# Optimization experiments

Hardware: AMD Instinct MI355X
Metric: run time of the kernel (lower is better)

The kernel has to match this reference:

```python
import jax, jax.numpy as jnp
import numpy as np

N_SRC, N_DST, N_EDGES = 60000, 50000, 600000
IN_DIM, OUT_DIM = 256, 128


def setup_inputs() -> dict:
    key = jax.random.key(0)
    k1, k2, k3, k4, k5, k6 = jax.random.split(key, 6)
    features = jax.random.normal(k1, (N_SRC, IN_DIM), dtype=jnp.float32)
    t = jax.random.uniform(k2, (N_SRC,), dtype=jnp.float32)
    edge_src = jax.random.randint(k3, (N_EDGES,), 0, N_SRC, dtype=jnp.int32)
    edge_dst = jax.random.randint(k4, (N_EDGES,), 0, N_DST, dtype=jnp.int32)
    # learned params: xavier_normal with relu gain for fc, default for temporal_fc
    gain = float(np.sqrt(2.0))
    std_fc = gain * np.sqrt(2.0 / (IN_DIM + OUT_DIM))
    W_fc = jax.random.normal(k5, (OUT_DIM, IN_DIM), dtype=jnp.float32) * std_fc
    W_t = jax.random.normal(k6, (1, OUT_DIM), dtype=jnp.float32) * (1.0 / np.sqrt(OUT_DIM))
    return {"features": features, "t": t, "edge_src": edge_src,
            "edge_dst": edge_dst, "n_dst": N_DST, "W_fc": W_fc, "W_t": W_t}


def reference(features, t, edge_src, edge_dst, n_dst, W_fc, W_t):
    # z = fc(h), no bias
    z = features @ W_fc.T                      # [n_src, out_dim]
    s = (z @ W_t.T)[:, 0]                      # temporal_fc(z) -> [n_src]
    # edge attention: e = -|t_src - t_dst| (non-differentiable in original)
    e = jax.lax.stop_gradient(-jnp.abs(t[edge_src] - t[edge_dst]))  # [E]
    # mailbox logits: exp(temporal_fc(z_src) * e / 500)
    y = jnp.exp(s[edge_src] * e / 500.0)       # [E]
    # segment softmax over incoming edges of each dst node
    m = jax.ops.segment_max(y, edge_dst, num_segments=n_dst)
    m = jnp.where(jnp.isfinite(m), m, 0.0)     # empty mailboxes
    ex = jnp.exp(y - m[edge_dst])
    denom = jax.ops.segment_sum(ex, edge_dst, num_segments=n_dst)
    alpha = ex / denom[edge_dst]               # [E]
    # weighted neighbor sum
    h = jax.ops.segment_sum(alpha[:, None] * z[edge_src], edge_dst, num_segments=n_dst)
    # residual
    return z[:n_dst] + h
```

## Files before the change

kernel.cpp:

```cpp
#include <hip/hip_runtime.h>
#include <cstdint>

#define NBINS 1024
#define EPB   4096
#define MAXE  1536

typedef __attribute__((ext_vector_type(8))) _Float16 half8;
typedef __attribute__((ext_vector_type(4))) float floatx4;

__device__ __forceinline__ half8 gload16(const void* p) {
    half8 v;
    asm volatile("global_load_dwordx4 %0, %1, off" : "=v"(v) : "v"(p));
    return v;
}

__global__ __launch_bounds__(512, 4) void gemm_hist(
    const float* __restrict__ A, const float* __restrict__ W,
    const float* __restrict__ Wt, const int* __restrict__ edst,
    _Float16* __restrict__ z16, float* __restrict__ s,
    int* __restrict__ gcount, int M, int E, int NBH)
{
    __shared__ __align__(16) unsigned char smem[65536];

    if ((int)blockIdx.x < NBH) {
        int* h = (int*)smem;
        for (int i = threadIdx.x; i < NBINS; i += 512) h[i] = 0;
        __syncthreads();
        int base = blockIdx.x * EPB + threadIdx.x * 8;
        if (base + 8 <= E) {
            int4 d0 = *(const int4*)(edst + base);
            int4 d1 = *(const int4*)(edst + base + 4);
            atomicAdd(&h[d0.x >> 6], 1); atomicAdd(&h[d0.y >> 6], 1);
            atomicAdd(&h[d0.z >> 6], 1); atomicAdd(&h[d0.w >> 6], 1);
            atomicAdd(&h[d1.x >> 6], 1); atomicAdd(&h[d1.y >> 6], 1);
            atomicAdd(&h[d1.z >> 6], 1); atomicAdd(&h[d1.w >> 6], 1);
        } else {
            for (int i = 0; i < 8; ++i)
                if (base + i < E) atomicAdd(&h[edst[base + i] >> 6], 1);
        }
        __syncthreads();
        for (int i = threadIdx.x; i < NBINS; i += 512)
            gcount[(size_t)blockIdx.x * NBINS + i] = h[i];
        return;
    }

    half8* Wlds = (half8*)smem;
    const int tile = blockIdx.x - NBH;
    const int tid  = threadIdx.x;
    const int lane = tid & 63;
    const int w    = tid >> 6;
    const int m    = lane & 15;
    const int q    = lane >> 4;

#pragma unroll
    for (int it = 0; it < 8; ++it) {
        int pair = w * 8 + it;
        int nt = pair & 7, ks = pair >> 3;
        const float* src = W + (size_t)(nt * 16 + m) * 256 + ks * 32 + q * 8;
        float4 w0 = *(const float4*)src;
        float4 w1 = *(const float4*)(src + 4);
        half8 h;
        h[0] = (_Float16)w0.x; h[1] = (_Float16)w0.y;
        h[2] = (_Float16)w0.z; h[3] = (_Float16)w0.w;
        h[4] = (_Float16)w1.x; h[5] = (_Float16)w1.y;
        h[6] = (_Float16)w1.z; h[7] = (_Float16)w1.w;
        Wlds[pair * 64 + lane] = h;
    }

    const int row_base = tile * 128 + w * 16;
    const int arow = min(row_base + m, M - 1);
    const float* ap = A + (size_t)arow * 256 + q * 8;

    float4 abuf[8];
#pragma unroll
    for (int i = 0; i < 4; ++i) {
        abuf[2 * i]     = *(const float4*)(ap + i * 32);
        abuf[2 * i + 1] = *(const float4*)(ap + i * 32 + 4);
    }

    floatx4 acc[8];
#pragma unroll
    for (int nt = 0; nt < 8; ++nt) acc[nt] = (floatx4){0.f, 0.f, 0.f, 0.f};

    __syncthreads();

#pragma unroll
    for (int ks = 0; ks < 8; ++ks) {
        float4 a0 = abuf[(ks & 3) * 2];
        float4 a1 = abuf[(ks & 3) * 2 + 1];
        half8 af;
        af[0] = (_Float16)a0.x; af[1] = (_Float16)a0.y;
        af[2] = (_Float16)a0.z; af[3] = (_Float16)a0.w;
        af[4] = (_Float16)a1.x; af[5] = (_Float16)a1.y;
        af[6] = (_Float16)a1.z; af[7] = (_Float16)a1.w;

        if (ks < 4) {
            abuf[(ks & 3) * 2]     = *(const float4*)(ap + (ks + 4) * 32);
            abuf[(ks & 3) * 2 + 1] = *(const float4*)(ap + (ks + 4) * 32 + 4);
        }

#pragma unroll
        for (int nt = 0; nt < 8; ++nt) {
            half8 bf = Wlds[(ks * 8 + nt) * 64 + lane];
            acc[nt] = __builtin_amdgcn_mfma_f32_16x16x32_f16(
                af, bf, acc[nt], 0, 0, 0);
        }
    }

    float wt[8];
#pragma unroll
    for (int nt = 0; nt < 8; ++nt) wt[nt] = Wt[nt * 16 + m];

    float sp[4] = {0.f, 0.f, 0.f, 0.f};
#pragma unroll
    for (int nt = 0; nt < 8; ++nt)
#pragma unroll
        for (int reg = 0; reg < 4; ++reg)
            sp[reg] += acc[nt][reg] * wt[nt];

#pragma unroll
    for (int reg = 0; reg < 4; ++reg) {
        int row = row_base + q * 4 + reg;
        if (row < M) {
#pragma unroll
            for (int nt = 0; nt < 8; ++nt)
                z16[(size_t)row * 128 + nt * 16 + m] = (_Float16)acc[nt][reg];
        }
    }
#pragma unroll
    for (int off = 1; off <= 8; off <<= 1)
#pragma unroll
        for (int reg = 0; reg < 4; ++reg)
            sp[reg] += __shfl_xor(sp[reg], off, 64);
    if (m == 0) {
#pragma unroll
        for (int reg = 0; reg < 4; ++reg) {
            int row = row_base + q * 4 + reg;
            if (row < M) s[row] = sp[reg];
        }
    }
}

__global__ __launch_bounds__(256) void part_scan(
    int* __restrict__ gcount, int* __restrict__ binTot, int NB)
{
    int b    = blockIdx.x * 4 + (threadIdx.x >> 6);
    int lane = threadIdx.x & 63;
    if (b >= NBINS) return;
    int chunks = (NB + 63) >> 6;
    int run = 0;
    for (int c = 0; c < chunks; ++c) {
        int blk = c * 64 + lane;
        int v = (blk < NB) ? gcount[(size_t)blk * NBINS + b] : 0;
        int incl = v;
#pragma unroll
        for (int off = 1; off < 64; off <<= 1) {
            int n = __shfl_up(incl, off, 64);
            if (lane >= off) incl += n;
        }
        if (blk < NB) gcount[(size_t)blk * NBINS + b] = run + incl - v;
        run += __shfl(incl, 63, 64);
    }
    if (lane == 0) binTot[b] = run;
}

__global__ __launch_bounds__(1024) void part_scanB(
    const int* __restrict__ binTot, int* __restrict__ binstart)
{
    __shared__ int wsum[16];
    int b = threadIdx.x;
    int lane = b & 63, wv = b >> 6;
    int v = binTot[b];
    int x = v;
#pragma unroll
    for (int off = 1; off < 64; off <<= 1) {
        int n = __shfl_up(x, off, 64);
        if (lane >= off) x += n;
    }
    if (lane == 63) wsum[wv] = x;
    __syncthreads();
    if (b < 64) {
        int t = (b < 16) ? wsum[b] : 0;
#pragma unroll
        for (int off = 1; off < 16; off <<= 1) {
            int n = __shfl_up(t, off, 64);
            if (lane >= off) t += n;
        }
        if (b < 16) wsum[b] = t;
    }
    __syncthreads();
    int base = (wv > 0) ? wsum[wv - 1] : 0;
    binstart[b] = base + x - v;
    if (b == NBINS - 1) binstart[NBINS] = base + x;
}

__global__ __launch_bounds__(512) void part_scatter(
    const int* __restrict__ esrc, const int* __restrict__ edst,
    const float* __restrict__ t, const float* __restrict__ s,
    const int* __restrict__ gcount, const int* __restrict__ binstart,
    int2* __restrict__ part, int E)
{
    __shared__ int hloc[NBINS];
    __shared__ int hbase[NBINS];
    for (int i = threadIdx.x; i < NBINS; i += 512) hloc[i] = 0;
    __syncthreads();

    int base = blockIdx.x * EPB + threadIdx.x * 8;
    int si[8], di[8], rk[8];
    int nv = 0;
    if (base < E) {
        nv = E - base; if (nv > 8) nv = 8;
        if (nv == 8) {
            int4 s0 = *(const int4*)(esrc + base);
            int4 s1 = *(const int4*)(esrc + base + 4);
            int4 d0 = *(const int4*)(edst + base);
            int4 d1 = *(const int4*)(edst + base + 4);
            si[0]=s0.x; si[1]=s0.y; si[2]=s0.z; si[3]=s0.w;
            si[4]=s1.x; si[5]=s1.y; si[6]=s1.z; si[7]=s1.w;
            di[0]=d0.x; di[1]=d0.y; di[2]=d0.z; di[3]=d0.w;
            di[4]=d1.x; di[5]=d1.y; di[6]=d1.z; di[7]=d1.w;
        } else {
            for (int i = 0; i < 8; ++i) {
                int e = min(base + i, E - 1);
                si[i] = esrc[e]; di[i] = edst[e];
            }
        }
#pragma unroll
        for (int i = 0; i < 8; ++i)
            if (i < nv) rk[i] = atomicAdd(&hloc[di[i] >> 6], 1);
    }

    for (int i = threadIdx.x; i < NBINS; i += 512)
        hbase[i] = binstart[i] + gcount[(size_t)blockIdx.x * NBINS + i];
    __syncthreads();

#pragma unroll
    for (int i = 0; i < 8; ++i) {
        if (i < nv) {
            float ee = -fabsf(t[si[i]] - t[di[i]]);
            float exv = __expf(__expf(s[si[i]] * ee * (1.0f / 500.0f)));
            part[hbase[di[i] >> 6] + rk[i]] =
                make_int2((si[i] & 0xffff) | ((di[i] & 63) << 16),
                          __float_as_int(exv));
        }
    }
}

__global__ __launch_bounds__(256) void aggregate(
    const _Float16* __restrict__ z16, const int* __restrict__ binstart,
    const int2* __restrict__ part, float* __restrict__ out, int Nd)
{
    __shared__ int2 arr[MAXE];
    __shared__ int lcnt[64];
    __shared__ int loff[65];

    const int tid = threadIdx.x;
    const int b = blockIdx.x;
    const int s0 = binstart[b];
    int nE = binstart[b + 1] - s0;
    if (nE > MAXE) nE = MAXE;

    if (tid < 64) lcnt[tid] = 0;
    __syncthreads();

    int2 rec[6]; int rrk[6], rloc[6], nrec = 0;
    for (int i = tid; i < nE; i += 256) {
        int2 r = part[s0 + i];
        int loc = (r.x >> 16) & 63;
        rec[nrec] = r;
        rloc[nrec] = loc;
        rrk[nrec] = atomicAdd(&lcnt[loc], 1);
        ++nrec;
    }
    __syncthreads();
    if (tid < 64) {
        int v = lcnt[tid], x = v;
#pragma unroll
        for (int off = 1; off < 64; off <<= 1) {
            int n = __shfl_up(x, off, 64);
            if (tid >= off) x += n;
        }
        loff[tid + 1] = x;
        if (tid == 0) loff[0] = 0;
    }
    __syncthreads();
    for (int i = 0; i < nrec; ++i)
        arr[loff[rloc[i]] + rrk[i]] = rec[i];
    __syncthreads();

    const int g = tid >> 4;
    const int l = tid & 15;

#pragma unroll 1
    for (int pass = 0; pass < 4; ++pass) {
        const int loc = pass * 16 + g;
        const int jb = loff[loc], je = loff[loc + 1];

        float acc[8];
#pragma unroll
        for (int i = 0; i < 8; ++i) acc[i] = 0.f;
        float ds = 0.f;

        for (int j = jb; j < je; j += 8) {
            float x[8];
            const void* p[8];
#pragma unroll
            for (int k = 0; k < 8; ++k) {
                bool vk = (j + k) < je;
                int jj = vk ? (j + k) : (je - 1);
                int2 r = arr[jj];
                x[k] = vk ? __int_as_float(r.y) : 0.f;
                p[k] = (const void*)(z16 + (size_t)(r.x & 0xffff) * 128 + l * 8);
            }
            half8 v0 = gload16(p[0]);
            half8 v1 = gload16(p[1]);
            half8 v2 = gload16(p[2]);
            half8 v3 = gload16(p[3]);
            half8 v4 = gload16(p[4]);
            half8 v5 = gload16(p[5]);
            half8 v6 = gload16(p[6]);
            half8 v7 = gload16(p[7]);
            asm volatile("s_waitcnt vmcnt(0)" ::: "memory");
            __builtin_amdgcn_sched_barrier(0);
            ds += ((x[0] + x[1]) + (x[2] + x[3])) +
                  ((x[4] + x[5]) + (x[6] + x[7]));
#pragma unroll
            for (int i = 0; i < 8; ++i) {
                acc[i] = fmaf(x[0], (float)v0[i], acc[i]);
                acc[i] = fmaf(x[1], (float)v1[i], acc[i]);
                acc[i] = fmaf(x[2], (float)v2[i], acc[i]);
                acc[i] = fmaf(x[3], (float)v3[i], acc[i]);
                acc[i] = fmaf(x[4], (float)v4[i], acc[i]);
                acc[i] = fmaf(x[5], (float)v5[i], acc[i]);
                acc[i] = fmaf(x[6], (float)v6[i], acc[i]);
                acc[i] = fmaf(x[7], (float)v7[i], acc[i]);
            }
        }

        int d = b * 64 + loc;
        if (d < Nd) {
            float inv = (je > jb) ? 1.0f / ds : 0.0f;
            const half8* zr = (const half8*)(z16 + (size_t)d * 128 + l * 8);
            half8 r0 = *zr;
            float* op = out + (size_t)d * 128 + l * 8;
            *(float4*)(op + 0) = make_float4(fmaf(acc[0], inv, (float)r0[0]),
                                             fmaf(acc[1], inv, (float)r0[1]),
                                             fmaf(acc[2], inv, (float)r0[2]),
                                             fmaf(acc[3], inv, (float)r0[3]));
            *(float4*)(op + 4) = make_float4(fmaf(acc[4], inv, (float)r0[4]),
                                             fmaf(acc[5], inv, (float)r0[5]),
                                             fmaf(acc[6], inv, (float)r0[6]),
                                             fmaf(acc[7], inv, (float)r0[7]));
        }
    }
}

extern "C" void kernel_launch(void* const* d_in, const int* in_sizes, int n_in,
                              void* d_out, int out_size, void* d_ws, size_t ws_size,
                              hipStream_t stream)
{
    const float* features = (const float*)d_in[0];
    const float* t        = (const float*)d_in[1];
    const int*   esrc     = (const int*)d_in[2];
    const int*   edst     = (const int*)d_in[3];
    const float* Wfc      = (const float*)d_in[5];
    const float* Wt       = (const float*)d_in[6];
    float* out = (float*)d_out;

    const int M  = in_sizes[1];
    const int E  = in_sizes[2];
    const int OD = in_sizes[6];
    const int Nd = out_size / OD;

    const int NBH = (E + EPB - 1) / EPB;
    const int GB  = (M + 127) / 128;

    _Float16* z16      = (_Float16*)d_ws;
    float*    s        = (float*)(z16 + (size_t)M * 128);
    int*      gcount   = (int*)(s + M);
    int*      binTot   = gcount + (size_t)NBH * NBINS;
    int*      binstart = binTot + NBINS;
    int2*     part     = (int2*)(binstart + NBINS + 4);

    gemm_hist<<<NBH + GB, 512, 0, stream>>>(features, Wfc, Wt, edst,
                                            z16, s, gcount, M, E, NBH);
    part_scan<<<NBINS / 4, 256, 0, stream>>>(gcount, binTot, NBH);
    part_scanB<<<1, 1024, 0, stream>>>(binTot, binstart);
    part_scatter<<<NBH, 512, 0, stream>>>(esrc, edst, t, s, gcount, binstart,
                                          part, E);
    aggregate<<<(Nd + 63) / 64, 256, 0, stream>>>(z16, binstart, part, out, Nd);
}
```

Measured before the change: 174.4 us.

## Split z16 into four column panels and process panels sequentially in aggregate

```diff
diff --git a/kernel.cpp b/kernel.cpp
--- a/kernel.cpp
+++ b/kernel.cpp
@@ -124,7 +124,8 @@
         if (row < M) {
 #pragma unroll
             for (int nt = 0; nt < 8; ++nt)
-                z16[(size_t)row * 128 + nt * 16 + m] = (_Float16)acc[nt][reg];
+                z16[(size_t)(nt >> 1) * (size_t)M * 32 +
+                    (size_t)row * 32 + (nt & 1) * 16 + m] = (_Float16)acc[nt][reg];
         }
     }
 #pragma unroll
@@ -248,7 +249,7 @@
 
 __global__ __launch_bounds__(256) void aggregate(
     const _Float16* __restrict__ z16, const int* __restrict__ binstart,
-    const int2* __restrict__ part, float* __restrict__ out, int Nd)
+    const int2* __restrict__ part, float* __restrict__ out, int M, int Nd)
 {
     __shared__ int2 arr[MAXE];
     __shared__ int lcnt[64];
@@ -288,42 +289,44 @@
         arr[loff[rloc[i]] + rrk[i]] = rec[i];
     __syncthreads();
 
-    const int g = tid >> 4;
-    const int l = tid & 15;
+    const int slot = tid >> 2;
+    const int f    = tid & 3;
+    const int jb = loff[slot], je = loff[slot + 1];
+    const int d  = b * 64 + slot;
+    float dsv = 0.f;
 
 #pragma unroll 1
-    for (int pass = 0; pass < 4; ++pass) {
-        const int loc = pass * 16 + g;
-        const int jb = loff[loc], je = loff[loc + 1];
+    for (int p = 0; p < 4; ++p) {
+        const _Float16* zp = z16 + (size_t)p * (size_t)M * 32;
 
         float acc[8];
 #pragma unroll
         for (int i = 0; i < 8; ++i) acc[i] = 0.f;
-        float ds = 0.f;
 
         for (int j = jb; j < je; j += 8) {
             float x[8];
-            const void* p[8];
+            const void* pp[8];
 #pragma unroll
             for (int k = 0; k < 8; ++k) {
                 bool vk = (j + k) < je;
                 int jj = vk ? (j + k) : (je - 1);
                 int2 r = arr[jj];
                 x[k] = vk ? __int_as_float(r.y) : 0.f;
-                p[k] = (const void*)(z16 + (size_t)(r.x & 0xffff) * 128 + l * 8);
+                pp[k] = (const void*)(zp + (size_t)(r.x & 0xffff) * 32 + f * 8);
             }
-            half8 v0 = gload16(p[0]);
-            half8 v1 = gload16(p[1]);
-            half8 v2 = gload16(p[2]);
-            half8 v3 = gload16(p[3]);
-            half8 v4 = gload16(p[4]);
-            half8 v5 = gload16(p[5]);
-            half8 v6 = gload16(p[6]);
-            half8 v7 = gload16(p[7]);
+            half8 v0 = gload16(pp[0]);
+            half8 v1 = gload16(pp[1]);
+            half8 v2 = gload16(pp[2]);
+            half8 v3 = gload16(pp[3]);
+            half8 v4 = gload16(pp[4]);
+            half8 v5 = gload16(pp[5]);
+            half8 v6 = gload16(pp[6]);
+            half8 v7 = gload16(pp[7]);
             asm volatile("s_waitcnt vmcnt(0)" ::: "memory");
             __builtin_amdgcn_sched_barrier(0);
-            ds += ((x[0] + x[1]) + (x[2] + x[3])) +
-                  ((x[4] + x[5]) + (x[6] + x[7]));
+            if (p == 0)
+                dsv += ((x[0] + x[1]) + (x[2] + x[3])) +
+                       ((x[4] + x[5]) + (x[6] + x[7]));
 #pragma unroll
             for (int i = 0; i < 8; ++i) {
                 acc[i] = fmaf(x[0], (float)v0[i], acc[i]);
@@ -337,12 +340,10 @@
             }
         }
 
-        int d = b * 64 + loc;
         if (d < Nd) {
-            float inv = (je > jb) ? 1.0f / ds : 0.0f;
-            const half8* zr = (const half8*)(z16 + (size_t)d * 128 + l * 8);
-            half8 r0 = *zr;
-            float* op = out + (size_t)d * 128 + l * 8;
+            float inv = (je > jb) ? 1.0f / dsv : 0.0f;
+            half8 r0 = *(const half8*)(zp + (size_t)d * 32 + f * 8);
+            float* op = out + (size_t)d * 128 + p * 32 + f * 8;
             *(float4*)(op + 0) = make_float4(fmaf(acc[0], inv, (float)r0[0]),
                                              fmaf(acc[1], inv, (float)r0[1]),
                                              fmaf(acc[2], inv, (float)r0[2]),
@@ -388,5 +389,6 @@
     part_scanB<<<1, 1024, 0, stream>>>(binTot, binstart);
     part_scatter<<<NBH, 512, 0, stream>>>(esrc, edst, t, s, gcount, binstart,
                                           part, E);
-    aggregate<<<(Nd + 63) / 64, 256, 0, stream>>>(z16, binstart, part, out, Nd);
-}
+    aggregate<<<(Nd + 63) / 64, 256, 0, stream>>>(z16, binstart, part, out,
+                                                  M, Nd);
+}
```

After: 178.2 us. 2.2% more time.
